# Performance work log

Measured on AMD Instinct MI355X. Metric: run time of the kernel, lower is better.

The kernel has to match this reference:

```python
import jax, jax.numpy as jnp
import numpy as np

BLOCK = (4, 4, 4)
NUM_HEADS = 8


def setup_inputs() -> dict:
    key = jax.random.key(0)
    ks = jax.random.split(key, 5)
    C = 128
    return {
        "x": jax.random.normal(ks[0], (2, C, 32, 62, 62), dtype=jnp.float32),
        "qkv_w": jax.random.normal(ks[1], (3 * C, C), dtype=jnp.float32) * 0.02,
        "qkv_b": jax.random.normal(ks[2], (3 * C,), dtype=jnp.float32) * 0.02,
        "conv_w": jax.random.normal(ks[3], (C, C, 1, 1, 1), dtype=jnp.float32) * 0.02,
        "conv_b": jax.random.normal(ks[4], (C,), dtype=jnp.float32) * 0.02,
    }


def reference(x, qkv_w, qkv_b, conv_w, conv_b):
    b0, b1, b2 = BLOCK
    heads = NUM_HEADS
    B, C, D, H0, W0 = x.shape
    pad_r = (-W0) % b2
    pad_b = (-H0) % b1
    x = jnp.pad(x, ((0, 0), (0, 0), (0, 0), (0, pad_b), (0, pad_r)))
    H, W = H0 + pad_b, W0 + pad_r
    d, h, w = D // b0, H // b1, W // b2
    hd = C // heads
    scale = hd ** (-0.5)
    T = b0 * b1 * b2  # tokens per 3D window
    nw = d * h * w    # number of windows

    # partition into windows: (B, nw, T, C)
    xw = x.reshape(B, C, d, b0, h, b1, w, b2).transpose(0, 2, 4, 6, 3, 5, 7, 1)
    xw = xw.reshape(B, nw, T, C)

    qkv = xw @ qkv_w.T + qkv_b  # (B, nw, T, 3C)
    qkv = qkv.reshape(B, nw, T, 3, heads, hd).transpose(3, 0, 1, 4, 2, 5)
    q, k, v = qkv[0], qkv[1], qkv[2]  # (B, nw, heads, T, hd)

    attn = jnp.einsum('bnhtc,bnhsc->bnhts', q, k) * scale

    if pad_r > 0 or pad_b > 0:
        mask = jnp.zeros((H, W), dtype=attn.dtype)
        if pad_b > 0:
            mask = mask.at[-pad_b:, :].set(1.0)
        if pad_r > 0:
            mask = mask.at[:, -pad_r:].set(1.0)
        # (h*w, b1*b2) per-2D-window pad flags
        mask = mask.reshape(h, b1, w, b2).transpose(0, 2, 1, 3).reshape(h * w, b1 * b2)
        am = mask[:, None, :] - mask[:, :, None]  # (h*w, b1*b2, b1*b2)
        am = jnp.where(am != 0, jnp.asarray(-1000.0, attn.dtype), jnp.asarray(0.0, attn.dtype))
        # tile over depth windows and depth tokens (matches torch .repeat)
        am = jnp.tile(am, (d, b0, b0))  # (nw, T, T)
        attn = attn + am[None, :, None, :, :]

    attn = jax.nn.softmax(attn, axis=-1)
    o = jnp.einsum('bnhts,bnhsc->bnhtc', attn, v)  # (B, nw, heads, T, hd)

    o = o.reshape(B, d, h, w, heads, b0, b1, b2, hd)
    o = o.transpose(0, 4, 8, 1, 5, 2, 6, 3, 7).reshape(B, C, D, H, W)
    o = o[:, :, :, :H0, :W0]

    # 1x1x1 Conv3d == channel mixing
    out = jnp.einsum('bcdhw,oc->bodhw', o, conv_w[:, :, 0, 0, 0])
    out = out + conv_b[None, :, None, None, None]
    return out
```

## Files before the change

### kernel.cpp

```cpp
#include <hip/hip_runtime.h>

typedef _Float16 f16x8 __attribute__((ext_vector_type(8)));
typedef _Float16 f16x4 __attribute__((ext_vector_type(4)));
typedef __fp16   fp16x2 __attribute__((ext_vector_type(2)));
typedef float    f32x4 __attribute__((ext_vector_type(4)));
typedef unsigned int u32x2 __attribute__((ext_vector_type(2)));

__device__ __forceinline__ f32x4 mfma32(f16x8 a, f16x8 b, f32x4 c) {
  return __builtin_amdgcn_mfma_f32_16x16x32_f16(a, b, c, 0, 0, 0);
}
__device__ __forceinline__ f32x4 mfma16(f16x4 a, f16x4 b, f32x4 c) {
#if __has_builtin(__builtin_amdgcn_mfma_f32_16x16x16f16)
  return __builtin_amdgcn_mfma_f32_16x16x16f16(a, b, c, 0, 0, 0);
#else
  f32x4 d;
  asm volatile("v_mfma_f32_16x16x16_f16 %0, %1, %2, %3"
               : "=v"(d) : "v"(a), "v"(b), "v"(c));
  return d;
#endif
}

__device__ __forceinline__ unsigned pk2(float a, float b) {
  union { fp16x2 h; unsigned u; } cv;
  cv.h = __builtin_amdgcn_cvt_pkrtz(a, b);
  return cv.u;
}

#define TR_READ(dst, addr, OFF) \
  asm volatile("ds_read_b64_tr_b16 %0, %1 offset:" OFF \
               : "=v"(dst) : "v"(addr) : "memory")

__global__ void cvt_weights(const float* __restrict__ qw, const float* __restrict__ cw,
                            _Float16* __restrict__ wq, _Float16* __restrict__ wc) {
  const int i = blockIdx.x * 256 + threadIdx.x;
  if (i < 384 * 128) wq[i] = (_Float16)qw[i];
  if (i < 128 * 128) wc[i] = (_Float16)cw[i];
}

__global__ void __launch_bounds__(512, 4)
win_attn(const float* __restrict__ xg, const _Float16* __restrict__ wq,
         const float* __restrict__ qbias, const _Float16* __restrict__ wc,
         const float* __restrict__ cb, float* __restrict__ outg)
{
  __shared__ char xsm[16384];
  __shared__ char wsm[8][6144];

  const int tid  = threadIdx.x;
  const int lane = tid & 63;
  const int wv   = tid >> 6;
  const int l15  = lane & 15;
  const int g    = lane >> 4;

  const int raw = blockIdx.x;
  const int wid = ((raw & 7) << 9) | (raw >> 3);
  const int ww = wid & 15, hh = (wid >> 4) & 15, dd = (wid >> 8) & 7, bb = wid >> 11;

  const f32x4 fz = {0.f, 0.f, 0.f, 0.f};

  {
    const int m4 = lane & 3, q4 = lane >> 2;
    const int i0 = q4 >> 2, i1 = q4 & 3;
    const int z = dd * 4 + i0, y = hh * 4 + i1;
    const bool yv   = (y < 62);
    const bool full = (ww < 15);
    float va[4][4];
#pragma unroll
    for (int it = 0; it < 4; ++it) {
      const int c = wv * 16 + it * 4 + m4;
      const float* src = xg + (((size_t)(bb * 128 + c) * 32 + (size_t)z) * 3844
                               + (size_t)(y * 62 + ww * 4));
      float a0 = 0.f, a1 = 0.f, a2 = 0.f, a3 = 0.f;
      if (yv) {
        const float2 lo = *reinterpret_cast<const float2*>(src);
        a0 = lo.x; a1 = lo.y;
        if (full) {
          const float2 hi = *reinterpret_cast<const float2*>(src + 2);
          a2 = hi.x; a3 = hi.y;
        }
      }
      va[it][0] = a0; va[it][1] = a1; va[it][2] = a2; va[it][3] = a3;
    }
#pragma unroll
    for (int it = 0; it < 4; ++it) {
      float v0 = va[it][0], v1 = va[it][1], v2 = va[it][2], v3 = va[it][3];
      float t0 = __shfl_xor((m4 & 1) ? v0 : v1, 1);
      float t1 = __shfl_xor((m4 & 1) ? v2 : v3, 1);
      if (m4 & 1) { v0 = t0; v2 = t1; } else { v1 = t0; v3 = t1; }
      float t2 = __shfl_xor((m4 & 2) ? v0 : v2, 2);
      float t3 = __shfl_xor((m4 & 2) ? v1 : v3, 2);
      if (m4 & 2) { v0 = t2; v1 = t3; } else { v2 = t2; v3 = t3; }
      f16x4 pk; pk[0] = (_Float16)v0; pk[1] = (_Float16)v1;
                pk[2] = (_Float16)v2; pk[3] = (_Float16)v3;
      const int c0 = wv * 16 + it * 4;
      *reinterpret_cast<f16x4*>(xsm + ((lane * 256 + 2 * c0) ^ ((lane & 15) << 4))) = pk;
    }
  }
  __syncthreads();

  char* sb = wsm[wv];
  const unsigned sb32 = (unsigned)(unsigned long long)sb;
  const unsigned trb  = sb32 + 8u * (unsigned)lane;
  const int vswz = (l15 & 7) << 4;

  unsigned long long pm = 0ull;
  if (hh == 15) pm |= 0xFF00FF00FF00FF00ull;
  if (ww == 15) pm |= 0xCCCCCCCCCCCCCCCCull;

  const float LOG2E = 1.4426950408889634f;
  const int swzA = l15 << 4;

#pragma unroll
  for (int co = 0; co < 3; ++co) {
    f32x4 acc[4] = {fz, fz, fz, fz};
    const int col = co * 128 + wv * 16 + l15;
#pragma unroll
    for (int kk = 0; kk < 4; ++kk) {
      const f16x8 bfr = *reinterpret_cast<const f16x8*>(wq + col * 128 + kk * 32 + g * 8);
#pragma unroll
      for (int ri = 0; ri < 4; ++ri) {
        const f16x8 a = *reinterpret_cast<const f16x8*>(
            xsm + (ri * 16 + l15) * 256 + ((kk * 64 + g * 16) ^ swzA));
        acc[ri] = mfma32(a, bfr, acc[ri]);
      }
    }
    const float bias = qbias[col];
    const float sc = (co == 0) ? 0.25f : 1.0f;
#pragma unroll
    for (int ri = 0; ri < 4; ++ri)
#pragma unroll
      for (int r = 0; r < 4; ++r) acc[ri][r] = (acc[ri][r] + bias) * sc;

    if (co == 2) {
#pragma unroll
      for (int ri = 0; ri < 4; ++ri) {
        const int s0 = ri * 16 + g * 4;
        *reinterpret_cast<unsigned*>(sb + 4096 + l15 * 128 + ((2 * s0) ^ vswz))
            = pk2(acc[ri][0], acc[ri][1]);
        *reinterpret_cast<unsigned*>(sb + 4096 + l15 * 128 + ((2 * (s0 + 2)) ^ vswz))
            = pk2(acc[ri][2], acc[ri][3]);
      }
    } else {
      const int base = (co == 0) ? 2048 : 0;
#pragma unroll
      for (int ri = 0; ri < 4; ++ri) {
        const int off = ri * 512 + l15 * 32 + g * 8;
        u32x2 w;
        w[0] = pk2(acc[ri][0], acc[ri][1]);
        w[1] = pk2(acc[ri][2], acc[ri][3]);
        *reinterpret_cast<u32x2*>(sb + base + off) = w;
      }
    }
  }
  asm volatile("s_waitcnt lgkmcnt(0)" ::: "memory");

  f16x4 ka[4], qa[4];
  TR_READ(ka[0], trb, "0");
  TR_READ(ka[1], trb, "512");
  TR_READ(ka[2], trb, "1024");
  TR_READ(ka[3], trb, "1536");
  TR_READ(qa[0], trb, "2048");
  TR_READ(qa[1], trb, "2560");
  TR_READ(qa[2], trb, "3072");
  TR_READ(qa[3], trb, "3584");
  f16x8 av0, av1;
  av0 = *reinterpret_cast<const f16x8*>(sb + 4096 + l15 * 128 + ((g * 16) ^ vswz));
  av1 = *reinterpret_cast<const f16x8*>(sb + 4096 + l15 * 128 + ((64 + g * 16) ^ vswz));
  asm volatile("s_waitcnt lgkmcnt(0)" ::: "memory");
  __builtin_amdgcn_sched_barrier(0);

  unsigned opk[4][2];
#pragma unroll
  for (int tjp = 0; tjp < 2; ++tjp) {
    const int tj0 = 2 * tjp, tj1 = 2 * tjp + 1;
    f32x4 st2[4][2];
#pragma unroll
    for (int si = 0; si < 4; ++si) {
      st2[si][0] = mfma16(ka[si], qa[tj0], fz);
      st2[si][1] = mfma16(ka[si], qa[tj1], fz);
    }

    if (pm) {
#pragma unroll
      for (int tjc = 0; tjc < 2; ++tjc) {
        const int t = (2 * tjp + tjc) * 16 + l15;
        const unsigned ft = (unsigned)(pm >> t) & 1u;
#pragma unroll
        for (int si = 0; si < 4; ++si)
#pragma unroll
          for (int r = 0; r < 4; ++r) {
            const int s = si * 16 + g * 4 + r;
            const unsigned fs = (unsigned)(pm >> s) & 1u;
            if (fs != ft) st2[si][tjc][r] -= 1000.f;
          }
      }
    }

#pragma unroll
    for (int tjc = 0; tjc < 2; ++tjc) {
      float mx = st2[0][tjc][0];
#pragma unroll
      for (int si = 0; si < 4; ++si)
#pragma unroll
        for (int r = 0; r < 4; ++r) mx = fmaxf(mx, st2[si][tjc][r]);
      mx = fmaxf(mx, __shfl_xor(mx, 16));
      mx = fmaxf(mx, __shfl_xor(mx, 32));
      float sum = 0.f;
#pragma unroll
      for (int si = 0; si < 4; ++si)
#pragma unroll
        for (int r = 0; r < 4; ++r) {
          const float e = __builtin_amdgcn_exp2f((st2[si][tjc][r] - mx) * LOG2E);
          st2[si][tjc][r] = e; sum += e;
        }
      sum += __shfl_xor(sum, 16);
      sum += __shfl_xor(sum, 32);
      const float inv = __builtin_amdgcn_rcpf(sum);
#pragma unroll
      for (int si = 0; si < 4; ++si)
#pragma unroll
        for (int r = 0; r < 4; ++r) st2[si][tjc][r] *= inv;
    }

#pragma unroll
    for (int tjc = 0; tjc < 2; ++tjc) {
      const int tl = tjc * 16 + l15;
#pragma unroll
      for (int si = 0; si < 4; ++si) {
        u32x2 w;
        w[0] = pk2(st2[si][tjc][0], st2[si][tjc][1]);
        w[1] = pk2(st2[si][tjc][2], st2[si][tjc][3]);
        *reinterpret_cast<u32x2*>(sb + tl * 128 + ((si * 32 + g * 8) ^ vswz)) = w;
      }
    }
    asm volatile("s_waitcnt lgkmcnt(0)" ::: "memory");

    f32x4 oa0 = fz, oa1 = fz;
    {
      const f16x8 pa00 = *reinterpret_cast<const f16x8*>(
          sb + l15 * 128 + ((g * 16) ^ vswz));
      const f16x8 pa10 = *reinterpret_cast<const f16x8*>(
          sb + (16 + l15) * 128 + ((g * 16) ^ vswz));
      oa0 = mfma32(av0, pa00, oa0);
      oa1 = mfma32(av0, pa10, oa1);
      const f16x8 pa01 = *reinterpret_cast<const f16x8*>(
          sb + l15 * 128 + ((64 + g * 16) ^ vswz));
      const f16x8 pa11 = *reinterpret_cast<const f16x8*>(
          sb + (16 + l15) * 128 + ((64 + g * 16) ^ vswz));
      oa0 = mfma32(av1, pa01, oa0);
      oa1 = mfma32(av1, pa11, oa1);
    }

    if (tjp == 0) {
      opk[0][0] = pk2(oa0[0], oa0[1]); opk[0][1] = pk2(oa0[2], oa0[3]);
      opk[1][0] = pk2(oa1[0], oa1[1]); opk[1][1] = pk2(oa1[2], oa1[3]);
    } else {
      opk[2][0] = pk2(oa0[0], oa0[1]); opk[2][1] = pk2(oa0[2], oa0[3]);
      opk[3][0] = pk2(oa1[0], oa1[1]); opk[3][1] = pk2(oa1[2], oa1[3]);
    }
    __builtin_amdgcn_sched_barrier(0);
  }
  __syncthreads();

#pragma unroll
  for (int tj = 0; tj < 4; ++tj) {
    const int t = tj * 16 + l15;
    u32x2 w0; w0[0] = opk[tj][0]; w0[1] = opk[tj][1];
    *reinterpret_cast<u32x2*>(xsm + t * 256 + ((wv * 32 + g * 8) ^ ((t & 15) << 4))) = w0;
  }
  __syncthreads();

  f32x4 cacc[4] = {fz, fz, fz, fz};
  const int cout = wv * 16 + l15;
#pragma unroll
  for (int kk = 0; kk < 4; ++kk) {
    const f16x8 bfr = *reinterpret_cast<const f16x8*>(wc + cout * 128 + kk * 32 + g * 8);
#pragma unroll
    for (int ri = 0; ri < 4; ++ri) {
      const f16x8 a = *reinterpret_cast<const f16x8*>(
          xsm + (ri * 16 + l15) * 256 + ((kk * 64 + g * 16) ^ swzA));
      cacc[ri] = mfma32(a, bfr, cacc[ri]);
    }
  }
  const int y = hh * 4 + g;
  if (y < 62) {
    const float bias = cb[cout];
#pragma unroll
    for (int ri = 0; ri < 4; ++ri) {
      const int z = dd * 4 + ri;
      float* dst = outg + (((size_t)(bb * 128 + cout) * 32 + (size_t)z) * 3844
                           + (size_t)(y * 62 + ww * 4));
      float2 lo; lo.x = cacc[ri][0] + bias; lo.y = cacc[ri][1] + bias;
      *reinterpret_cast<float2*>(dst) = lo;
      if (ww < 15) {
        float2 hi; hi.x = cacc[ri][2] + bias; hi.y = cacc[ri][3] + bias;
        *reinterpret_cast<float2*>(dst + 2) = hi;
      }
    }
  }
}

extern "C" void kernel_launch(void* const* d_in, const int* in_sizes, int n_in,
                              void* d_out, int out_size, void* d_ws, size_t ws_size,
                              hipStream_t stream) {
  const float* x  = (const float*)d_in[0];
  const float* qw = (const float*)d_in[1];
  const float* qb = (const float*)d_in[2];
  const float* cw = (const float*)d_in[3];
  const float* cb = (const float*)d_in[4];
  float* out = (float*)d_out;

  if (ws_size < (size_t)(384 * 128 + 128 * 128) * sizeof(_Float16)) return;
  _Float16* wq = (_Float16*)d_ws;
  _Float16* wc = wq + 384 * 128;

  cvt_weights<<<192, 256, 0, stream>>>(qw, cw, wq, wc);
  win_attn<<<4096, 512, 0, stream>>>(x, wq, qb, wc, cb, out);
}
```

Measured before the change: 173.3 us.

## Build V operand via cross-lane shuffles instead of LDS to shrink shared memory

The V projection results are no longer written to per-wave LDS and read back. They are packed to fp16 and redistributed into the MFMA A-operand layout with __shfl and lane selects. The per-wave LDS scratch shrinks from 6144 to 4096 bytes and the launch-bounds occupancy hint rises from 4 to 6, aiming to fit more blocks per CU and cut LDS traffic. The bias and scale step is fused into the pack step, and one sched_barrier is removed. The trade-off is extra shuffle instructions and a tighter register budget that could cause spills.

```diff
diff --git a/kernel.cpp b/kernel.cpp
--- a/kernel.cpp
+++ b/kernel.cpp
@@ -37,13 +37,13 @@
   if (i < 128 * 128) wc[i] = (_Float16)cw[i];
 }
 
-__global__ void __launch_bounds__(512, 4)
+__global__ void __launch_bounds__(512, 6)
 win_attn(const float* __restrict__ xg, const _Float16* __restrict__ wq,
          const float* __restrict__ qbias, const _Float16* __restrict__ wc,
          const float* __restrict__ cb, float* __restrict__ outg)
 {
   __shared__ char xsm[16384];
-  __shared__ char wsm[8][6144];
+  __shared__ char wsm[8][4096];
 
   const int tid  = threadIdx.x;
   const int lane = tid & 63;
@@ -109,6 +109,8 @@
   const float LOG2E = 1.4426950408889634f;
   const int swzA = l15 << 4;
 
+  f16x8 av0, av1;
+
 #pragma unroll
   for (int co = 0; co < 3; ++co) {
     f32x4 acc[4] = {fz, fz, fz, fz};
@@ -124,29 +126,53 @@
       }
     }
     const float bias = qbias[col];
-    const float sc = (co == 0) ? 0.25f : 1.0f;
-#pragma unroll
-    for (int ri = 0; ri < 4; ++ri)
-#pragma unroll
-      for (int r = 0; r < 4; ++r) acc[ri][r] = (acc[ri][r] + bias) * sc;
 
     if (co == 2) {
+      unsigned vp[4][2];
 #pragma unroll
       for (int ri = 0; ri < 4; ++ri) {
-        const int s0 = ri * 16 + g * 4;
-        *reinterpret_cast<unsigned*>(sb + 4096 + l15 * 128 + ((2 * s0) ^ vswz))
-            = pk2(acc[ri][0], acc[ri][1]);
-        *reinterpret_cast<unsigned*>(sb + 4096 + l15 * 128 + ((2 * (s0 + 2)) ^ vswz))
-            = pk2(acc[ri][2], acc[ri][3]);
+        vp[ri][0] = pk2(acc[ri][0] + bias, acc[ri][1] + bias);
+        vp[ri][1] = pk2(acc[ri][2] + bias, acc[ri][3] + bias);
+      }
+      const int srcA = l15 + 32 * (g & 1);
+      const bool hi = (g >= 2);
+      {
+        const unsigned a0 = __shfl(vp[0][0], srcA);
+        const unsigned a1 = __shfl(vp[0][1], srcA);
+        const unsigned a2 = __shfl(vp[0][0], srcA + 16);
+        const unsigned a3 = __shfl(vp[0][1], srcA + 16);
+        const unsigned b0 = __shfl(vp[1][0], srcA);
+        const unsigned b1 = __shfl(vp[1][1], srcA);
+        const unsigned b2 = __shfl(vp[1][0], srcA + 16);
+        const unsigned b3 = __shfl(vp[1][1], srcA + 16);
+        union { unsigned w[4]; f16x8 v; } u;
+        u.w[0] = hi ? b0 : a0; u.w[1] = hi ? b1 : a1;
+        u.w[2] = hi ? b2 : a2; u.w[3] = hi ? b3 : a3;
+        av0 = u.v;
+      }
+      {
+        const unsigned a0 = __shfl(vp[2][0], srcA);
+        const unsigned a1 = __shfl(vp[2][1], srcA);
+        const unsigned a2 = __shfl(vp[2][0], srcA + 16);
+        const unsigned a3 = __shfl(vp[2][1], srcA + 16);
+        const unsigned b0 = __shfl(vp[3][0], srcA);
+        const unsigned b1 = __shfl(vp[3][1], srcA);
+        const unsigned b2 = __shfl(vp[3][0], srcA + 16);
+        const unsigned b3 = __shfl(vp[3][1], srcA + 16);
+        union { unsigned w[4]; f16x8 v; } u;
+        u.w[0] = hi ? b0 : a0; u.w[1] = hi ? b1 : a1;
+        u.w[2] = hi ? b2 : a2; u.w[3] = hi ? b3 : a3;
+        av1 = u.v;
       }
     } else {
       const int base = (co == 0) ? 2048 : 0;
+      const float sc = (co == 0) ? 0.25f : 1.0f;
 #pragma unroll
       for (int ri = 0; ri < 4; ++ri) {
         const int off = ri * 512 + l15 * 32 + g * 8;
         u32x2 w;
-        w[0] = pk2(acc[ri][0], acc[ri][1]);
-        w[1] = pk2(acc[ri][2], acc[ri][3]);
+        w[0] = pk2((acc[ri][0] + bias) * sc, (acc[ri][1] + bias) * sc);
+        w[1] = pk2((acc[ri][2] + bias) * sc, (acc[ri][3] + bias) * sc);
         *reinterpret_cast<u32x2*>(sb + base + off) = w;
       }
     }
@@ -162,9 +188,6 @@
   TR_READ(qa[1], trb, "2560");
   TR_READ(qa[2], trb, "3072");
   TR_READ(qa[3], trb, "3584");
-  f16x8 av0, av1;
-  av0 = *reinterpret_cast<const f16x8*>(sb + 4096 + l15 * 128 + ((g * 16) ^ vswz));
-  av1 = *reinterpret_cast<const f16x8*>(sb + 4096 + l15 * 128 + ((64 + g * 16) ^ vswz));
   asm volatile("s_waitcnt lgkmcnt(0)" ::: "memory");
   __builtin_amdgcn_sched_barrier(0);
 
@@ -257,7 +280,6 @@
       opk[2][0] = pk2(oa0[0], oa0[1]); opk[2][1] = pk2(oa0[2], oa0[3]);
       opk[3][0] = pk2(oa1[0], oa1[1]); opk[3][1] = pk2(oa1[2], oa1[3]);
     }
-    __builtin_amdgcn_sched_barrier(0);
   }
   __syncthreads();
 
```

After: 391.0 us. +125.6%, slower.

## Keep P in registers via lane shuffles, defer softmax normalization, add obuf

Applied to the files above, without the earlier changes.

The softmax probabilities are no longer written to and re-read from per-wave LDS. The PV MFMA operands are now assembled from registers with cross-lane shuffles, and the 1/sum normalization moves onto the output instead of each probability. LOG2E is folded into the Q scale so the exponent skips a multiply. A separate LDS output buffer replaces reuse of xsm, which removes one __syncthreads, and s_setprio hints wrap the MFMA loops. In exchange it adds 32 shuffles per PV tile and 16KB more LDS, which may lower occupancy.

```diff
diff --git a/kernel.cpp b/kernel.cpp
--- a/kernel.cpp
+++ b/kernel.cpp
@@ -43,6 +43,7 @@
          const float* __restrict__ cb, float* __restrict__ outg)
 {
   __shared__ char xsm[16384];
+  __shared__ char obuf[16384];
   __shared__ char wsm[8][6144];
 
   const int tid  = threadIdx.x;
@@ -106,13 +107,13 @@
   if (hh == 15) pm |= 0xFF00FF00FF00FF00ull;
   if (ww == 15) pm |= 0xCCCCCCCCCCCCCCCCull;
 
-  const float LOG2E = 1.4426950408889634f;
   const int swzA = l15 << 4;
 
 #pragma unroll
   for (int co = 0; co < 3; ++co) {
     f32x4 acc[4] = {fz, fz, fz, fz};
     const int col = co * 128 + wv * 16 + l15;
+    __builtin_amdgcn_s_setprio(1);
 #pragma unroll
     for (int kk = 0; kk < 4; ++kk) {
       const f16x8 bfr = *reinterpret_cast<const f16x8*>(wq + col * 128 + kk * 32 + g * 8);
@@ -123,30 +124,27 @@
         acc[ri] = mfma32(a, bfr, acc[ri]);
       }
     }
+    __builtin_amdgcn_s_setprio(0);
     const float bias = qbias[col];
-    const float sc = (co == 0) ? 0.25f : 1.0f;
-#pragma unroll
-    for (int ri = 0; ri < 4; ++ri)
-#pragma unroll
-      for (int r = 0; r < 4; ++r) acc[ri][r] = (acc[ri][r] + bias) * sc;
 
     if (co == 2) {
 #pragma unroll
       for (int ri = 0; ri < 4; ++ri) {
         const int s0 = ri * 16 + g * 4;
         *reinterpret_cast<unsigned*>(sb + 4096 + l15 * 128 + ((2 * s0) ^ vswz))
-            = pk2(acc[ri][0], acc[ri][1]);
+            = pk2(acc[ri][0] + bias, acc[ri][1] + bias);
         *reinterpret_cast<unsigned*>(sb + 4096 + l15 * 128 + ((2 * (s0 + 2)) ^ vswz))
-            = pk2(acc[ri][2], acc[ri][3]);
+            = pk2(acc[ri][2] + bias, acc[ri][3] + bias);
       }
     } else {
       const int base = (co == 0) ? 2048 : 0;
+      const float sc = (co == 0) ? 0.25f * 1.4426950408889634f : 1.0f;
 #pragma unroll
       for (int ri = 0; ri < 4; ++ri) {
         const int off = ri * 512 + l15 * 32 + g * 8;
         u32x2 w;
-        w[0] = pk2(acc[ri][0], acc[ri][1]);
-        w[1] = pk2(acc[ri][2], acc[ri][3]);
+        w[0] = pk2((acc[ri][0] + bias) * sc, (acc[ri][1] + bias) * sc);
+        w[1] = pk2((acc[ri][2] + bias) * sc, (acc[ri][3] + bias) * sc);
         *reinterpret_cast<u32x2*>(sb + base + off) = w;
       }
     }
@@ -168,7 +166,10 @@
   asm volatile("s_waitcnt lgkmcnt(0)" ::: "memory");
   __builtin_amdgcn_sched_barrier(0);
 
-  unsigned opk[4][2];
+  const int src0 = ((g & 1) << 5) + l15;
+  const int src1 = src0 + 16;
+  const bool ghi = (g >= 2);
+
 #pragma unroll
   for (int tjp = 0; tjp < 2; ++tjp) {
     const int tj0 = 2 * tjp, tj1 = 2 * tjp + 1;
@@ -195,6 +196,7 @@
       }
     }
 
+    float invs[2];
 #pragma unroll
     for (int tjc = 0; tjc < 2; ++tjc) {
       float mx = st2[0][tjc][0];
@@ -209,78 +211,80 @@
       for (int si = 0; si < 4; ++si)
 #pragma unroll
         for (int r = 0; r < 4; ++r) {
-          const float e = __builtin_amdgcn_exp2f((st2[si][tjc][r] - mx) * LOG2E);
+          const float e = __builtin_amdgcn_exp2f(st2[si][tjc][r] - mx);
           st2[si][tjc][r] = e; sum += e;
         }
       sum += __shfl_xor(sum, 16);
       sum += __shfl_xor(sum, 32);
-      const float inv = __builtin_amdgcn_rcpf(sum);
-#pragma unroll
-      for (int si = 0; si < 4; ++si)
-#pragma unroll
-        for (int r = 0; r < 4; ++r) st2[si][tjc][r] *= inv;
-    }
-
-#pragma unroll
-    for (int tjc = 0; tjc < 2; ++tjc) {
-      const int tl = tjc * 16 + l15;
-#pragma unroll
-      for (int si = 0; si < 4; ++si) {
-        u32x2 w;
-        w[0] = pk2(st2[si][tjc][0], st2[si][tjc][1]);
-        w[1] = pk2(st2[si][tjc][2], st2[si][tjc][3]);
-        *reinterpret_cast<u32x2*>(sb + tl * 128 + ((si * 32 + g * 8) ^ vswz)) = w;
-      }
-    }
-    asm volatile("s_waitcnt lgkmcnt(0)" ::: "memory");
+      invs[tjc] = __builtin_amdgcn_rcpf(sum);
+    }
+
+    unsigned plo[4][2], phi[4][2];
+#pragma unroll
+    for (int si = 0; si < 4; ++si)
+#pragma unroll
+      for (int tjc = 0; tjc < 2; ++tjc) {
+        plo[si][tjc] = pk2(st2[si][tjc][0], st2[si][tjc][1]);
+        phi[si][tjc] = pk2(st2[si][tjc][2], st2[si][tjc][3]);
+      }
+
+#define BUILD_PA(KC, TJC, DST)                                            \
+    {                                                                     \
+      const unsigned a0 = __shfl(plo[2*(KC)    ][TJC], src0);             \
+      const unsigned a1 = __shfl(phi[2*(KC)    ][TJC], src0);             \
+      const unsigned a2 = __shfl(plo[2*(KC)    ][TJC], src1);             \
+      const unsigned a3 = __shfl(phi[2*(KC)    ][TJC], src1);             \
+      const unsigned b0 = __shfl(plo[2*(KC) + 1][TJC], src0);             \
+      const unsigned b1 = __shfl(phi[2*(KC) + 1][TJC], src0);             \
+      const unsigned b2 = __shfl(plo[2*(KC) + 1][TJC], src1);             \
+      const unsigned b3 = __shfl(phi[2*(KC) + 1][TJC], src1);             \
+      union { unsigned w[4]; f16x8 v; } u;                                \
+      u.w[0] = ghi ? b0 : a0; u.w[1] = ghi ? b1 : a1;                     \
+      u.w[2] = ghi ? b2 : a2; u.w[3] = ghi ? b3 : a3;                     \
+      DST = u.v;                                                          \
+    }
 
     f32x4 oa0 = fz, oa1 = fz;
     {
-      const f16x8 pa00 = *reinterpret_cast<const f16x8*>(
-          sb + l15 * 128 + ((g * 16) ^ vswz));
-      const f16x8 pa10 = *reinterpret_cast<const f16x8*>(
-          sb + (16 + l15) * 128 + ((g * 16) ^ vswz));
-      oa0 = mfma32(av0, pa00, oa0);
-      oa1 = mfma32(av0, pa10, oa1);
-      const f16x8 pa01 = *reinterpret_cast<const f16x8*>(
-          sb + l15 * 128 + ((64 + g * 16) ^ vswz));
-      const f16x8 pa11 = *reinterpret_cast<const f16x8*>(
-          sb + (16 + l15) * 128 + ((64 + g * 16) ^ vswz));
-      oa0 = mfma32(av1, pa01, oa0);
-      oa1 = mfma32(av1, pa11, oa1);
-    }
-
-    if (tjp == 0) {
-      opk[0][0] = pk2(oa0[0], oa0[1]); opk[0][1] = pk2(oa0[2], oa0[3]);
-      opk[1][0] = pk2(oa1[0], oa1[1]); opk[1][1] = pk2(oa1[2], oa1[3]);
-    } else {
-      opk[2][0] = pk2(oa0[0], oa0[1]); opk[2][1] = pk2(oa0[2], oa0[3]);
-      opk[3][0] = pk2(oa1[0], oa1[1]); opk[3][1] = pk2(oa1[2], oa1[3]);
-    }
-    __builtin_amdgcn_sched_barrier(0);
-  }
-  __syncthreads();
-
-#pragma unroll
-  for (int tj = 0; tj < 4; ++tj) {
-    const int t = tj * 16 + l15;
-    u32x2 w0; w0[0] = opk[tj][0]; w0[1] = opk[tj][1];
-    *reinterpret_cast<u32x2*>(xsm + t * 256 + ((wv * 32 + g * 8) ^ ((t & 15) << 4))) = w0;
+      f16x8 pa;
+      __builtin_amdgcn_s_setprio(1);
+      BUILD_PA(0, 0, pa); oa0 = mfma32(av0, pa, oa0);
+      BUILD_PA(1, 0, pa); oa0 = mfma32(av1, pa, oa0);
+      BUILD_PA(0, 1, pa); oa1 = mfma32(av0, pa, oa1);
+      BUILD_PA(1, 1, pa); oa1 = mfma32(av1, pa, oa1);
+      __builtin_amdgcn_s_setprio(0);
+    }
+#undef BUILD_PA
+
+    {
+      const int t0 = tj0 * 16 + l15;
+      u32x2 w0;
+      w0[0] = pk2(oa0[0] * invs[0], oa0[1] * invs[0]);
+      w0[1] = pk2(oa0[2] * invs[0], oa0[3] * invs[0]);
+      *reinterpret_cast<u32x2*>(obuf + t0 * 256 + ((wv * 32 + g * 8) ^ ((t0 & 15) << 4))) = w0;
+      const int t1 = tj1 * 16 + l15;
+      u32x2 w1;
+      w1[0] = pk2(oa1[0] * invs[1], oa1[1] * invs[1]);
+      w1[1] = pk2(oa1[2] * invs[1], oa1[3] * invs[1]);
+      *reinterpret_cast<u32x2*>(obuf + t1 * 256 + ((wv * 32 + g * 8) ^ ((t1 & 15) << 4))) = w1;
+    }
   }
   __syncthreads();
 
   f32x4 cacc[4] = {fz, fz, fz, fz};
   const int cout = wv * 16 + l15;
+  __builtin_amdgcn_s_setprio(1);
 #pragma unroll
   for (int kk = 0; kk < 4; ++kk) {
     const f16x8 bfr = *reinterpret_cast<const f16x8*>(wc + cout * 128 + kk * 32 + g * 8);
 #pragma unroll
     for (int ri = 0; ri < 4; ++ri) {
       const f16x8 a = *reinterpret_cast<const f16x8*>(
-          xsm + (ri * 16 + l15) * 256 + ((kk * 64 + g * 16) ^ swzA));
+          obuf + (ri * 16 + l15) * 256 + ((kk * 64 + g * 16) ^ swzA));
       cacc[ri] = mfma32(a, bfr, cacc[ri]);
     }
   }
+  __builtin_amdgcn_s_setprio(0);
   const int y = hh * 4 + g;
   if (y < 62) {
     const float bias = cb[cout];
```

New measurement: 189.8 us. 1.1x slower.
